# Performance work log

Hardware: AMD Instinct MI355X
Metric: run time of the kernel (lower is better)

Reference implementation:

```python
import jax, jax.numpy as jnp
import numpy as np

INF = 1e8
EPS = 1e-6
STRIDES = (8, 16, 32, 64, 128)
FEAT_SIZES = ((100, 128), (50, 64), (25, 32), (13, 16), (7, 8))
NUM_CLASSES = 81  # args.num_classes + 1
BG = NUM_CLASSES
TOPK1, TOPK2 = 3, 1
RATIO = 0.9
FRACTION = 0.5
B, G = 16, 32
NPER = [h * w for h, w in FEAT_SIZES]
OFFS = np.cumsum([0] + NPER)


def gen_trf():
    j = [2 ** i for i in range(8)]
    r1 = 1 + 6 * j[0]; r2 = r1 + 2 * j[1]
    p2 = r2 + 2 * j[2] * 3; r3 = p2 + 2 * j[2]
    p3 = r3 + 2 * j[3] * 3; r4 = p3 + 2 * j[3]
    p4 = r4 + 2 * j[4] * 5; r5 = p4 + 2 * j[4]
    p5 = r5 + 2 * j[5] * 2
    p6 = p5 + 2 * j[6]; p7 = p6 + 2 * j[7]
    return [p2, p3, p4, p5, p6, p7]


def make_points_rfields():
    trfs = gen_trf()
    pts, rfs = [], []
    for lvl, (h, w) in enumerate(FEAT_SIZES):
        s = STRIDES[lvl]
        xs = jnp.arange(w, dtype=jnp.float32) * s + s // 2
        ys = jnp.arange(h, dtype=jnp.float32) * s + s // 2
        Y, X = jnp.meshgrid(ys, xs, indexing='ij')
        p = jnp.stack([X.reshape(-1), Y.reshape(-1)], -1)
        pts.append(p)
        rf = trfs[lvl + 1] * FRACTION  # fpn_layer == 'p3' -> rfnum = lvl + 1
        rfs.append(jnp.concatenate([p - rf / 2, p + rf / 2], -1))
    return jnp.concatenate(pts, 0), jnp.concatenate(rfs, 0)


def kl_overlaps(gts, anc):
    # BboxDistanceMetric mode='kl': Gaussian KL divergence -> 1/(1+kl); (G, N)
    c1 = (gts[:, :2] + gts[:, 2:]) / 2
    c2 = (anc[:, :2] + anc[:, 2:]) / 2
    w1 = gts[:, 2] - gts[:, 0] + EPS; h1 = gts[:, 3] - gts[:, 1] + EPS
    w2 = anc[:, 2] - anc[:, 0] + EPS; h2 = anc[:, 3] - anc[:, 1] + EPS
    dx = c1[:, None, 0] - c2[None, :, 0]; dy = c1[:, None, 1] - c2[None, :, 1]
    w1s = (w1 ** 2)[:, None]; h1s = (h1 ** 2)[:, None]
    w2s = (w2 ** 2)[None, :]; h2s = (h2 ** 2)[None, :]
    kl = (w2s / w1s + h2s / h1s + 4 * dx ** 2 / w1s + 4 * dy ** 2 / h1s
          + jnp.log(w1s / w2s) + jnp.log(h1s / h2s) - 2) / 2
    return 1.0 / (1.0 + kl)


def hie_assign(rf1, rf2, gts):
    ov1 = kl_overlaps(gts, rf1)
    ov2 = kl_overlaps(gts, rf2)
    N = rf1.shape[0]; Gn = gts.shape[0]
    max_ov = ov1.max(0)
    assigned = jnp.where((max_ov >= 0) & (max_ov < 0.8), 0, -1).astype(jnp.int32)
    gt_ids = jnp.arange(1, Gn + 1, dtype=jnp.int32)
    _, i1 = jax.lax.top_k(ov1, TOPK1)  # (G, k1)
    s1 = jnp.full((N,), -1, jnp.int32).at[i1.reshape(-1)].max(jnp.repeat(gt_ids, TOPK1))
    assigned = jnp.where(s1 > 0, s1, assigned)
    _, i2 = jax.lax.top_k(ov2, TOPK2)  # (G, k2) second hierarchy overrides
    s2 = jnp.full((N,), -1, jnp.int32).at[i2.reshape(-1)].max(jnp.repeat(gt_ids, TOPK2))
    return jnp.where(s2 > 0, s2, assigned)


def target_single(gts, glabels, points, rf1, rf2):
    Gn = gts.shape[0]
    assigned = hie_assign(rf1, rf2, gts)  # (N,) 1-based gt index, 0/-1 = bg
    areas = (gts[:, 2] - gts[:, 0]) * (gts[:, 3] - gts[:, 1])
    mask = (assigned - 1)[:, None] == jnp.arange(Gn)[None, :]
    am = jnp.where(mask, areas[None, :], INF)
    min_area = am.min(1); mi = jnp.argmin(am, 1)
    lab = jnp.where(min_area >= INF, BG, glabels[mi])
    g = gts[mi]
    bt = jnp.stack([points[:, 0] - g[:, 0], points[:, 1] - g[:, 1],
                    g[:, 2] - points[:, 0], g[:, 3] - points[:, 1]], -1)
    return lab, bt


def diou_loss(pred, tgt):
    lt = jnp.maximum(pred[:, :2], tgt[:, :2])
    rb = jnp.minimum(pred[:, 2:], tgt[:, 2:])
    wh = jnp.clip(rb - lt, 0.0)
    ov = wh[:, 0] * wh[:, 1]
    ap = (pred[:, 2] - pred[:, 0]) * (pred[:, 3] - pred[:, 1])
    ag = (tgt[:, 2] - tgt[:, 0]) * (tgt[:, 3] - tgt[:, 1])
    ious = ov / (ap + ag - ov + EPS)
    elt = jnp.minimum(pred[:, :2], tgt[:, :2])
    erb = jnp.maximum(pred[:, 2:], tgt[:, 2:])
    ewh = jnp.clip(erb - elt, 0.0)
    c2 = ewh[:, 0] ** 2 + ewh[:, 1] ** 2 + EPS
    rho2 = ((pred[:, 0] + pred[:, 2] - tgt[:, 0] - tgt[:, 2]) ** 2
            + (pred[:, 1] + pred[:, 3] - tgt[:, 1] - tgt[:, 3]) ** 2) / 4
    return 1.0 - (ious - rho2 / c2)


def _forward(cls_l, bbox_l, ctr_l, gt_bboxes, gt_labels):
    points, rf1 = make_points_rfields()
    c = (rf1[:, :2] + rf1[:, 2:]) / 2
    wh = (rf1[:, 2:] - rf1[:, :2]) * RATIO
    rf2 = jnp.concatenate([c - wh / 2, c + wh / 2], -1)
    labels_all, targets_all = jax.vmap(target_single, (0, 0, None, None, None))(
        gt_bboxes, gt_labels, points, rf1, rf2)
    labels_all = jax.lax.stop_gradient(labels_all)
    targets_all = jax.lax.stop_gradient(targets_all)
    # flatten level-major, image-minor (matches torch.cat order in loss)
    fc = jnp.concatenate([t.transpose(0, 2, 3, 1).reshape(-1, NUM_CLASSES) for t in cls_l], 0)
    fb = jnp.concatenate([t.transpose(0, 2, 3, 1).reshape(-1, 4) for t in bbox_l], 0)
    fo = jnp.concatenate([t.transpose(0, 2, 3, 1).reshape(-1) for t in ctr_l], 0)
    fl = jnp.concatenate([labels_all[:, OFFS[i]:OFFS[i + 1]].reshape(-1) for i in range(5)], 0)
    ft = jnp.concatenate([targets_all[:, OFFS[i]:OFFS[i + 1]].reshape(-1, 4) for i in range(5)], 0)
    fp = jnp.concatenate([jnp.tile(points[OFFS[i]:OFFS[i + 1]], (B, 1)) for i in range(5)], 0)
    pos = fl < BG
    posf = pos.astype(fc.dtype)
    num_pos = jnp.maximum(posf.sum(), 1.0)
    # sigmoid focal loss (alpha=0.25, gamma=2); bg label -> all-zero one-hot
    tgt = jax.nn.one_hot(fl, NUM_CLASSES, dtype=fc.dtype)
    p = jax.nn.sigmoid(fc)
    pt = (1 - p) * tgt + p * (1 - tgt)
    fw = (0.25 * tgt + 0.75 * (1 - tgt)) * pt ** 2
    bce = jnp.maximum(fc, 0) - fc * tgt + jnp.log1p(jnp.exp(-jnp.abs(fc)))
    loss_cls = (bce * fw).sum() / num_pos
    # centerness target (sanitized on negatives to avoid nan)
    bt = jnp.where(pos[:, None], ft, 1.0)
    lr_min = jnp.minimum(bt[:, 0], bt[:, 2]); lr_max = jnp.maximum(bt[:, 0], bt[:, 2])
    tb_min = jnp.minimum(bt[:, 1], bt[:, 3]); tb_max = jnp.maximum(bt[:, 1], bt[:, 3])
    ctr_tgt = jnp.sqrt(jnp.clip((lr_min / lr_max) * (tb_min / tb_max), 0.0)) * posf
    denom = jnp.maximum(ctr_tgt.sum(), 1e-6)
    # decode distances to boxes and DIoU loss weighted by centerness
    x, y = fp[:, 0], fp[:, 1]
    pb = jnp.stack([x - fb[:, 0], y - fb[:, 1], x + fb[:, 2], y + fb[:, 3]], -1)
    tb_box = jnp.stack([x - bt[:, 0], y - bt[:, 1], x + bt[:, 2], y + bt[:, 3]], -1)
    loss_bbox = (diou_loss(pb, tb_box) * ctr_tgt).sum() / denom
    # centerness BCE-with-logits, averaged by num_pos
    bce_c = jnp.maximum(fo, 0) - fo * ctr_tgt + jnp.log1p(jnp.exp(-jnp.abs(fo)))
    loss_ctr = (bce_c * posf).sum() / num_pos
    return jnp.stack([loss_cls, loss_bbox, loss_ctr])


def setup_inputs() -> dict:
    key = jax.random.key(0)
    ks = jax.random.split(key, 24)
    cls_l = [jax.random.normal(ks[i], (B, NUM_CLASSES, h, w), jnp.float32) - 4.0
             for i, (h, w) in enumerate(FEAT_SIZES)]
    bbox_l = [jax.random.uniform(ks[5 + i], (B, 4, h, w), jnp.float32) * 64.0 + 1.0
              for i, (h, w) in enumerate(FEAT_SIZES)]
    ctr_l = [jax.random.normal(ks[10 + i], (B, 1, h, w), jnp.float32)
             for i, (h, w) in enumerate(FEAT_SIZES)]
    cx = jax.random.uniform(ks[15], (B, G)) * 1000.0 + 12.0
    cy = jax.random.uniform(ks[16], (B, G)) * 776.0 + 12.0
    w = jax.random.uniform(ks[17], (B, G)) * 240.0 + 8.0
    h = jax.random.uniform(ks[18], (B, G)) * 240.0 + 8.0
    gt_bboxes = jnp.stack([cx - w / 2, cy - h / 2, cx + w / 2, cy + h / 2], -1)
    gt_labels = jax.random.randint(ks[19], (B, G), 0, 80)
    d = {}
    for i in range(5):
        d[f'cls{i}'] = cls_l[i]; d[f'bbox{i}'] = bbox_l[i]; d[f'ctr{i}'] = ctr_l[i]
    d['gt_bboxes'] = gt_bboxes
    d['gt_labels'] = gt_labels
    return d


def reference(cls0, cls1, cls2, cls3, cls4, bbox0, bbox1, bbox2, bbox3, bbox4,
              ctr0, ctr1, ctr2, ctr3, ctr4, gt_bboxes, gt_labels):
    return _forward([cls0, cls1, cls2, cls3, cls4],
                    [bbox0, bbox1, bbox2, bbox3, bbox4],
                    [ctr0, ctr1, ctr2, ctr3, ctr4], gt_bboxes, gt_labels)
```

## Files before the change

kernel.cpp:

```cpp
#include <hip/hip_runtime.h>
#include <math.h>
#include <limits.h>

#pragma clang fp contract(off)

#define N_ANCH 17064
#define BATCH  16
#define NGT    32
#define BG_CLS 81
#define EPSF   1e-6f

#define NPB     512
#define NSTREAM 2048
#define L2E 1.44269504088896340736f
#define LN2 0.69314718055994530942f

#define F4_0 4147200
#define C1   4147200
#define C2   5184000
#define C3   5443200
#define C4   5510592
#define TOT4 5528736

__device__ __forceinline__ float fexp2(float x){ return __builtin_amdgcn_exp2f(x); }
__device__ __forceinline__ float flog2(float x){ return __builtin_amdgcn_logf(x); }
__device__ __forceinline__ float frcp (float x){ return __builtin_amdgcn_rcpf(x); }

struct Geo { int lvl; int j; int HW; float px; float py; };

__device__ __forceinline__ Geo geom(int n) {
  Geo g;
  if (n < 12800)      { g.lvl=0; g.j=n;       g.HW=12800; g.px=(float)((g.j & 127)*8 + 4);   g.py=(float)((g.j >> 7)*8 + 4);   }
  else if (n < 16000) { g.lvl=1; g.j=n-12800; g.HW=3200;  g.px=(float)((g.j & 63)*16 + 8);   g.py=(float)((g.j >> 6)*16 + 8);  }
  else if (n < 16800) { g.lvl=2; g.j=n-16000; g.HW=800;   g.px=(float)((g.j & 31)*32 + 16);  g.py=(float)((g.j >> 5)*32 + 16); }
  else if (n < 17008) { g.lvl=3; g.j=n-16800; g.HW=208;   g.px=(float)((g.j & 15)*64 + 32);  g.py=(float)((g.j >> 4)*64 + 32); }
  else                { g.lvl=4; g.j=n-17008; g.HW=56;    g.px=(float)((g.j & 7)*128 + 64);  g.py=(float)((g.j >> 3)*128 + 64);}
  return g;
}

__device__ __forceinline__ bool bet(float av, int ai, float bv, int bi) {
  return (av < bv) || (av == bv && ai < bi);
}

__device__ __forceinline__ void insert3min(float* v, int* i, float nv, int ni) {
  if (nv < v[0])      { v[2]=v[1]; i[2]=i[1]; v[1]=v[0]; i[1]=i[0]; v[0]=nv; i[0]=ni; }
  else if (nv < v[1]) { v[2]=v[1]; i[2]=i[1]; v[1]=nv; i[1]=ni; }
  else                { v[2]=nv; i[2]=ni; }
}

__device__ __forceinline__ void insert3tie(float* v, int* i, float nv, int ni) {
  if (!bet(nv, ni, v[2], i[2])) return;
  if (bet(nv, ni, v[0], i[0]))      { v[2]=v[1]; i[2]=i[1]; v[1]=v[0]; i[1]=i[0]; v[0]=nv; i[0]=ni; }
  else if (bet(nv, ni, v[1], i[1])) { v[2]=v[1]; i[2]=i[1]; v[1]=nv; i[1]=ni; }
  else                              { v[2]=nv; i[2]=ni; }
}

__device__ __forceinline__ float negterm(float x) {
  float ax = fabsf(x);
  float e  = fexp2(ax * -L2E);
  float r  = frcp(1.0f + e);
  float p  = (x >= 0.0f) ? r : e * r;
  float sp = fmaxf(x, 0.0f) + flog2(1.0f + e) * LN2;
  return 0.75f * (p * p) * sp;
}

__global__ __launch_bounds__(256) void megaK(const float4* __restrict__ gtb,
                                             const float4* __restrict__ s0,
                                             const float4* __restrict__ s1,
                                             const float4* __restrict__ s2,
                                             const float4* __restrict__ s3,
                                             const float4* __restrict__ s4,
                                             int4* __restrict__ win,
                                             float* __restrict__ part) {
  __shared__ float sv[256 * 3];
  __shared__ int   si[256 * 3];
  __shared__ float tv[256];
  __shared__ int   ti[256];
  __shared__ float sh[256];

  int t = threadIdx.x;
  if (blockIdx.x < NPB) {
    int blk = blockIdx.x;
    int b = blk >> 5, g = blk & 31;
    float4 GB = gtb[b * NGT + g];
    float c1x = (GB.x + GB.z) * 0.5f, c1y = (GB.y + GB.w) * 0.5f;
    float w1 = GB.z - GB.x + EPSF, h1 = GB.w - GB.y + EPSF;
    float w1s = w1 * w1, h1s = h1 * h1;
    float iw = 1.0f / w1s, ih = 1.0f / h1s;
    float iws = iw + ih;
    float Lg = logf(w1s) + logf(h1s);
    float Ay = 4.0f * ih;
    float Axc = 4.0f * iw;

    float v1[3] = {INFINITY, INFINITY, INFINITY};
    int   i1[3] = {INT_MAX, INT_MAX, INT_MAX};
    float v2 = INFINITY; int i2 = INT_MAX;

    #define DO_LEVEL(BASE, LGW, H, STRIDE, RF) do {                             \
      const int W_ = 1 << (LGW);                                                \
      float w2a = (RF) + 1e-6f;          float w2sa = w2a * w2a;                \
      float w2b = (RF) * 0.9f + 1e-6f;   float w2sb = w2b * w2b;                \
      float K1 = w2sa * iws + Lg - 2.0f * logf(w2sa) - 2.0f;                    \
      float K2 = w2sb * iws + Lg - 2.0f * logf(w2sb) - 2.0f;                    \
      int col = t & (W_ - 1);                                                   \
      float px = (float)(col * (STRIDE) + (STRIDE) / 2);                        \
      float dx = c1x - px;                                                      \
      float kx1 = Axc * dx * dx + K1;                                           \
      float kx2 = Axc * dx * dx + K2;                                           \
      int rstep = 256 >> (LGW);                                                 \
      for (int row = t >> (LGW); row < (H); row += rstep) {                     \
        float py = (float)(row * (STRIDE) + (STRIDE) / 2);                      \
        float dy = c1y - py;                                                    \
        float dy2 = dy * dy;                                                    \
        float k1 = fmaf(Ay, dy2, kx1);                                          \
        float k2 = fmaf(Ay, dy2, kx2);                                          \
        int n = (BASE) + (row << (LGW)) + col;                                  \
        if (k1 < v1[2]) insert3min(v1, i1, k1, n);                              \
        if (k2 < v2) { v2 = k2; i2 = n; }                                       \
      }                                                                         \
    } while (0)

    DO_LEVEL(0,     7, 100,   8,  45.5f);
    DO_LEVEL(12800, 6,  50,  16, 133.5f);
    DO_LEVEL(16000, 5,  25,  32, 213.5f);
    DO_LEVEL(16800, 4,  13,  64, 277.5f);
    DO_LEVEL(17008, 3,   7, 128, 405.5f);
    #undef DO_LEVEL

    sv[t*3+0] = v1[0]; sv[t*3+1] = v1[1]; sv[t*3+2] = v1[2];
    si[t*3+0] = i1[0]; si[t*3+1] = i1[1]; si[t*3+2] = i1[2];
    tv[t] = v2; ti[t] = i2;
    __syncthreads();
    for (int off = 128; off > 0; off >>= 1) {
      if (t < off) {
        #pragma unroll
        for (int k = 0; k < 3; ++k)
          insert3tie(&sv[t * 3], &si[t * 3], sv[(t + off) * 3 + k], si[(t + off) * 3 + k]);
        if (bet(tv[t + off], ti[t + off], tv[t], ti[t])) { tv[t] = tv[t + off]; ti[t] = ti[t + off]; }
      }
      __syncthreads();
    }
    if (t == 0) win[blk] = make_int4(si[0], si[1], si[2], ti[0]);
  } else {
    int sb = blockIdx.x - NPB;
    float local = 0.0f;
    for (int i = sb * 256 + t; i < TOT4; i += NSTREAM * 256) {
      const float4* p; int off;
      if (i < C1)      { p = s0; off = i; }
      else if (i < C2) { p = s1; off = i - C1; }
      else if (i < C3) { p = s2; off = i - C2; }
      else if (i < C4) { p = s3; off = i - C3; }
      else             { p = s4; off = i - C4; }
      float4 f = p[off];
      local += negterm(f.x);
      local += negterm(f.y);
      local += negterm(f.z);
      local += negterm(f.w);
    }
    sh[t] = local;
    __syncthreads();
    #pragma unroll
    for (int off = 128; off > 0; off >>= 1) {
      if (t < off) sh[t] += sh[t + off];
      __syncthreads();
    }
    if (t == 0) part[sb] = sh[0];
  }
}

__global__ __launch_bounds__(1024) void resolveK(
    const int* __restrict__ win, const float4* __restrict__ gtb, const int* __restrict__ glab,
    const float* __restrict__ c0, const float* __restrict__ c1, const float* __restrict__ c2,
    const float* __restrict__ c3, const float* __restrict__ c4,
    const float* __restrict__ bb0, const float* __restrict__ bb1, const float* __restrict__ bb2,
    const float* __restrict__ bb3, const float* __restrict__ bb4,
    const float* __restrict__ ct0, const float* __restrict__ ct1, const float* __restrict__ ct2,
    const float* __restrict__ ct3, const float* __restrict__ ct4,
    const float* __restrict__ part, float* __restrict__ out) {
  int t = threadIdx.x;
  __shared__ unsigned int keys[NPB * 4];
  for (int k = t; k < NPB * 4; k += 1024) {
    int blk = k >> 2, s = k & 3;
    int b = blk >> 5, g = blk & 31;
    int n = win[k];
    unsigned int pri = ((s == 3) ? 32u : 0u) + (unsigned int)g;
    keys[k] = (((unsigned int)(b * 32768 + n)) << 6) | pri;
  }
  __syncthreads();

  double a_cls = 0.0, a_pos = 0.0, a_ctr = 0.0, a_diou = 0.0, a_cbce = 0.0;

  for (int i = t; i < NSTREAM; i += 1024) a_cls += (double)part[i];

  const float* clsA[5] = {c0, c1, c2, c3, c4};
  const float* bbA[5]  = {bb0, bb1, bb2, bb3, bb4};
  const float* ctA[5]  = {ct0, ct1, ct2, ct3, ct4};

  for (int k = t; k < NPB * 4; k += 1024) {
    unsigned int me = keys[k];
    unsigned int bn = me >> 6;
    int b = (int)(bn >> 15);
    int base = b * 128;
    bool alive = true;
    #pragma unroll 4
    for (int j = 0; j < 128; ++j) {
      unsigned int o = keys[base + j];
      if ((o >> 6) == bn && o > me) { alive = false; }
    }
    if (!alive) continue;

    int n = (int)(bn & 32767u);
    int g = (int)(me & 31u);
    int lab = glab[b * NGT + g];
    float4 gb = gtb[b * NGT + g];
    Geo G = geom(n);

    const float* bb = bbA[G.lvl];
    const float* ct = ctA[G.lvl];
    const float* cp = clsA[G.lvl];

    const float* bp = bb + b * 4 * G.HW + G.j;
    float f0 = bp[0];
    float f1 = bp[G.HW];
    float f2 = bp[2 * G.HW];
    float f3 = bp[3 * G.HW];
    float fo = ct[b * G.HW + G.j];
    float xc = cp[((size_t)(b * 81 + lab)) * G.HW + G.j];

    {
      float ax = fabsf(xc);
      float e  = fexp2(ax * -L2E);
      float r  = frcp(1.0f + e);
      float p  = (xc >= 0.0f) ? r : e * r;
      float sp = fmaxf(xc, 0.0f) + flog2(1.0f + e) * LN2;
      float neg = 0.75f * (p * p) * sp;
      float omp = 1.0f - p;
      float pos = 0.25f * (omp * omp) * (sp - xc);
      a_cls += (double)(pos - neg);
    }

    float tx = G.px - gb.x, ty = G.py - gb.y, tz = gb.z - G.px, tw = gb.w - G.py;

    float lr_min = fminf(tx, tz), lr_max = fmaxf(tx, tz);
    float tb_min = fminf(ty, tw), tb_max = fmaxf(ty, tw);
    float prod = (lr_min / lr_max) * (tb_min / tb_max);
    float ctrt = sqrtf(fmaxf(prod, 0.0f));

    float pb0 = G.px - f0, pb1 = G.py - f1, pb2 = G.px + f2, pb3 = G.py + f3;
    float tb0 = G.px - tx, tb1 = G.py - ty, tb2 = G.px + tz, tb3 = G.py + tw;

    float ltx = fmaxf(pb0, tb0), lty = fmaxf(pb1, tb1);
    float rbx = fminf(pb2, tb2), rby = fminf(pb3, tb3);
    float whx = fmaxf(rbx - ltx, 0.0f), why = fmaxf(rby - lty, 0.0f);
    float ovl = whx * why;
    float ap = (pb2 - pb0) * (pb3 - pb1);
    float ag = (tb2 - tb0) * (tb3 - tb1);
    float ious = ovl / (ap + ag - ovl + EPSF);
    float eltx = fminf(pb0, tb0), elty = fminf(pb1, tb1);
    float erbx = fmaxf(pb2, tb2), erby = fmaxf(pb3, tb3);
    float ewx = fmaxf(erbx - eltx, 0.0f), ewy = fmaxf(erby - elty, 0.0f);
    float c2v = ewx * ewx + ewy * ewy + EPSF;
    float sx = pb0 + pb2 - tb0 - tb2;
    float sy = pb1 + pb3 - tb1 - tb3;
    float rho2 = (sx * sx + sy * sy) * 0.25f;
    float dl = 1.0f - (ious - rho2 / c2v);

    a_pos  += 1.0;
    a_ctr  += (double)ctrt;
    a_diou += (double)(dl * ctrt);
    a_cbce += (double)(fmaxf(fo, 0.0f) - fo * ctrt + log1pf(expf(-fabsf(fo))));
  }

  __shared__ double r0[1024], r1[1024], r2[1024], r3[1024], r4[1024];
  r0[t] = a_cls; r1[t] = a_pos; r2[t] = a_ctr; r3[t] = a_diou; r4[t] = a_cbce;
  __syncthreads();
  #pragma unroll
  for (int off = 512; off > 0; off >>= 1) {
    if (t < off) {
      r0[t] += r0[t + off]; r1[t] += r1[t + off]; r2[t] += r2[t + off];
      r3[t] += r3[t + off]; r4[t] += r4[t + off];
    }
    __syncthreads();
  }
  if (t == 0) {
    double np_ = r1[0] > 1.0 ? r1[0] : 1.0;
    double dn  = r2[0] > 1e-6 ? r2[0] : 1e-6;
    out[0] = (float)(r0[0] / np_);
    out[1] = (float)(r3[0] / dn);
    out[2] = (float)(r4[0] / np_);
  }
}

extern "C" void kernel_launch(void* const* d_in, const int* in_sizes, int n_in,
                              void* d_out, int out_size, void* d_ws, size_t ws_size,
                              hipStream_t stream) {
  (void)in_sizes; (void)n_in; (void)out_size; (void)ws_size;
  const float* cls[5] = {(const float*)d_in[0],  (const float*)d_in[3],  (const float*)d_in[6],
                         (const float*)d_in[9],  (const float*)d_in[12]};
  const float* bbx[5] = {(const float*)d_in[1],  (const float*)d_in[4],  (const float*)d_in[7],
                         (const float*)d_in[10], (const float*)d_in[13]};
  const float* ctr[5] = {(const float*)d_in[2],  (const float*)d_in[5],  (const float*)d_in[8],
                         (const float*)d_in[11], (const float*)d_in[14]};
  const float4* gtb = (const float4*)d_in[15];
  const int* glab = (const int*)d_in[16];

  char* ws = (char*)d_ws;
  int4*  win  = (int4*)ws;
  float* part = (float*)(ws + NPB * 16);

  megaK<<<NPB + NSTREAM, 256, 0, stream>>>(gtb,
                                           (const float4*)cls[0], (const float4*)cls[1],
                                           (const float4*)cls[2], (const float4*)cls[3],
                                           (const float4*)cls[4],
                                           win, part);
  resolveK<<<1, 1024, 0, stream>>>((const int*)win, gtb, glab,
                                   cls[0], cls[1], cls[2], cls[3], cls[4],
                                   bbx[0], bbx[1], bbx[2], bbx[3], bbx[4],
                                   ctr[0], ctr[1], ctr[2], ctr[3], ctr[4],
                                   part, (float*)d_out);
}
```

Measured before the change: 42.79 us.

## Split resolve kernel into per-batch blocks with last-block final reduction

The single 1024-thread resolve kernel is replaced by one 256-thread block per batch image. Each block deduplicates its own 128 winner keys and computes the positive-anchor losses, then publishes per-batch partial sums through atomics. A done-counter, reset inside the first kernel, lets the last finishing block sum the stream partials and write the final outputs. This spreads the serial resolve work across several compute units, at the cost of atomic coordination and a counter-ordering dependency between the two kernels.

```diff
diff --git a/kernel.cpp b/kernel.cpp
--- a/kernel.cpp
+++ b/kernel.cpp
@@ -15,7 +15,6 @@
 #define L2E 1.44269504088896340736f
 #define LN2 0.69314718055994530942f
 
-#define F4_0 4147200
 #define C1   4147200
 #define C2   5184000
 #define C3   5443200
@@ -71,7 +70,8 @@
                                              const float4* __restrict__ s3,
                                              const float4* __restrict__ s4,
                                              int4* __restrict__ win,
-                                             float* __restrict__ part) {
+                                             float* __restrict__ part,
+                                             int* __restrict__ done) {
   __shared__ float sv[256 * 3];
   __shared__ int   si[256 * 3];
   __shared__ float tv[256];
@@ -79,6 +79,8 @@
   __shared__ float sh[256];
 
   int t = threadIdx.x;
+  if (blockIdx.x == 0 && t == 0) *done = 0;
+
   if (blockIdx.x < NPB) {
     int blk = blockIdx.x;
     int b = blk >> 5, g = blk & 31;
@@ -168,7 +170,7 @@
   }
 }
 
-__global__ __launch_bounds__(1024) void resolveK(
+__global__ __launch_bounds__(256) void resolveK(
     const int* __restrict__ win, const float4* __restrict__ gtb, const int* __restrict__ glab,
     const float* __restrict__ c0, const float* __restrict__ c1, const float* __restrict__ c2,
     const float* __restrict__ c3, const float* __restrict__ c4,
@@ -176,118 +178,150 @@
     const float* __restrict__ bb3, const float* __restrict__ bb4,
     const float* __restrict__ ct0, const float* __restrict__ ct1, const float* __restrict__ ct2,
     const float* __restrict__ ct3, const float* __restrict__ ct4,
-    const float* __restrict__ part, float* __restrict__ out) {
+    const float* __restrict__ part,
+    unsigned long long* __restrict__ bpart,
+    int* __restrict__ done,
+    float* __restrict__ out) {
   int t = threadIdx.x;
-  __shared__ unsigned int keys[NPB * 4];
-  for (int k = t; k < NPB * 4; k += 1024) {
-    int blk = k >> 2, s = k & 3;
-    int b = blk >> 5, g = blk & 31;
-    int n = win[k];
+  int b = blockIdx.x;
+  __shared__ unsigned int ukeys[128];
+
+  if (t < 128) {
+    int g = t >> 2, s = t & 3;
+    int n = win[(b * NGT + g) * 4 + s];
     unsigned int pri = ((s == 3) ? 32u : 0u) + (unsigned int)g;
-    keys[k] = (((unsigned int)(b * 32768 + n)) << 6) | pri;
+    ukeys[t] = (((unsigned int)n) << 6) | pri;
   }
   __syncthreads();
 
   double a_cls = 0.0, a_pos = 0.0, a_ctr = 0.0, a_diou = 0.0, a_cbce = 0.0;
-
-  for (int i = t; i < NSTREAM; i += 1024) a_cls += (double)part[i];
 
   const float* clsA[5] = {c0, c1, c2, c3, c4};
   const float* bbA[5]  = {bb0, bb1, bb2, bb3, bb4};
   const float* ctA[5]  = {ct0, ct1, ct2, ct3, ct4};
 
-  for (int k = t; k < NPB * 4; k += 1024) {
-    unsigned int me = keys[k];
-    unsigned int bn = me >> 6;
-    int b = (int)(bn >> 15);
-    int base = b * 128;
+  if (t < 128) {
+    unsigned int me = ukeys[t];
+    unsigned int nn = me >> 6;
     bool alive = true;
-    #pragma unroll 4
+    #pragma unroll 8
     for (int j = 0; j < 128; ++j) {
-      unsigned int o = keys[base + j];
-      if ((o >> 6) == bn && o > me) { alive = false; }
-    }
-    if (!alive) continue;
-
-    int n = (int)(bn & 32767u);
-    int g = (int)(me & 31u);
-    int lab = glab[b * NGT + g];
-    float4 gb = gtb[b * NGT + g];
-    Geo G = geom(n);
-
-    const float* bb = bbA[G.lvl];
-    const float* ct = ctA[G.lvl];
-    const float* cp = clsA[G.lvl];
-
-    const float* bp = bb + b * 4 * G.HW + G.j;
-    float f0 = bp[0];
-    float f1 = bp[G.HW];
-    float f2 = bp[2 * G.HW];
-    float f3 = bp[3 * G.HW];
-    float fo = ct[b * G.HW + G.j];
-    float xc = cp[((size_t)(b * 81 + lab)) * G.HW + G.j];
-
-    {
-      float ax = fabsf(xc);
-      float e  = fexp2(ax * -L2E);
-      float r  = frcp(1.0f + e);
-      float p  = (xc >= 0.0f) ? r : e * r;
-      float sp = fmaxf(xc, 0.0f) + flog2(1.0f + e) * LN2;
-      float neg = 0.75f * (p * p) * sp;
-      float omp = 1.0f - p;
-      float pos = 0.25f * (omp * omp) * (sp - xc);
-      a_cls += (double)(pos - neg);
-    }
-
-    float tx = G.px - gb.x, ty = G.py - gb.y, tz = gb.z - G.px, tw = gb.w - G.py;
-
-    float lr_min = fminf(tx, tz), lr_max = fmaxf(tx, tz);
-    float tb_min = fminf(ty, tw), tb_max = fmaxf(ty, tw);
-    float prod = (lr_min / lr_max) * (tb_min / tb_max);
-    float ctrt = sqrtf(fmaxf(prod, 0.0f));
-
-    float pb0 = G.px - f0, pb1 = G.py - f1, pb2 = G.px + f2, pb3 = G.py + f3;
-    float tb0 = G.px - tx, tb1 = G.py - ty, tb2 = G.px + tz, tb3 = G.py + tw;
-
-    float ltx = fmaxf(pb0, tb0), lty = fmaxf(pb1, tb1);
-    float rbx = fminf(pb2, tb2), rby = fminf(pb3, tb3);
-    float whx = fmaxf(rbx - ltx, 0.0f), why = fmaxf(rby - lty, 0.0f);
-    float ovl = whx * why;
-    float ap = (pb2 - pb0) * (pb3 - pb1);
-    float ag = (tb2 - tb0) * (tb3 - tb1);
-    float ious = ovl / (ap + ag - ovl + EPSF);
-    float eltx = fminf(pb0, tb0), elty = fminf(pb1, tb1);
-    float erbx = fmaxf(pb2, tb2), erby = fmaxf(pb3, tb3);
-    float ewx = fmaxf(erbx - eltx, 0.0f), ewy = fmaxf(erby - elty, 0.0f);
-    float c2v = ewx * ewx + ewy * ewy + EPSF;
-    float sx = pb0 + pb2 - tb0 - tb2;
-    float sy = pb1 + pb3 - tb1 - tb3;
-    float rho2 = (sx * sx + sy * sy) * 0.25f;
-    float dl = 1.0f - (ious - rho2 / c2v);
-
-    a_pos  += 1.0;
-    a_ctr  += (double)ctrt;
-    a_diou += (double)(dl * ctrt);
-    a_cbce += (double)(fmaxf(fo, 0.0f) - fo * ctrt + log1pf(expf(-fabsf(fo))));
-  }
-
-  __shared__ double r0[1024], r1[1024], r2[1024], r3[1024], r4[1024];
+      unsigned int o = ukeys[j];
+      if ((o >> 6) == nn && o > me) alive = false;
+    }
+    if (alive) {
+      int n = (int)nn;
+      int g = (int)(me & 31u);
+      int lab = glab[b * NGT + g];
+      float4 gb = gtb[b * NGT + g];
+      Geo G = geom(n);
+
+      const float* bb = bbA[G.lvl];
+      const float* ct = ctA[G.lvl];
+      const float* cp = clsA[G.lvl];
+
+      const float* bp = bb + b * 4 * G.HW + G.j;
+      float f0 = bp[0];
+      float f1 = bp[G.HW];
+      float f2 = bp[2 * G.HW];
+      float f3 = bp[3 * G.HW];
+      float fo = ct[b * G.HW + G.j];
+      float xc = cp[((size_t)(b * 81 + lab)) * G.HW + G.j];
+
+      {
+        float ax = fabsf(xc);
+        float e  = fexp2(ax * -L2E);
+        float r  = frcp(1.0f + e);
+        float p  = (xc >= 0.0f) ? r : e * r;
+        float sp = fmaxf(xc, 0.0f) + flog2(1.0f + e) * LN2;
+        float neg = 0.75f * (p * p) * sp;
+        float omp = 1.0f - p;
+        float pos = 0.25f * (omp * omp) * (sp - xc);
+        a_cls += (double)(pos - neg);
+      }
+
+      float tx = G.px - gb.x, ty = G.py - gb.y, tz = gb.z - G.px, tw = gb.w - G.py;
+
+      float lr_min = fminf(tx, tz), lr_max = fmaxf(tx, tz);
+      float tb_min = fminf(ty, tw), tb_max = fmaxf(ty, tw);
+      float prod = (lr_min / lr_max) * (tb_min / tb_max);
+      float ctrt = sqrtf(fmaxf(prod, 0.0f));
+
+      float pb0 = G.px - f0, pb1 = G.py - f1, pb2 = G.px + f2, pb3 = G.py + f3;
+      float tb0 = G.px - tx, tb1 = G.py - ty, tb2 = G.px + tz, tb3 = G.py + tw;
+
+      float ltx = fmaxf(pb0, tb0), lty = fmaxf(pb1, tb1);
+      float rbx = fminf(pb2, tb2), rby = fminf(pb3, tb3);
+      float whx = fmaxf(rbx - ltx, 0.0f), why = fmaxf(rby - lty, 0.0f);
+      float ovl = whx * why;
+      float ap = (pb2 - pb0) * (pb3 - pb1);
+      float ag = (tb2 - tb0) * (tb3 - tb1);
+      float ious = ovl / (ap + ag - ovl + EPSF);
+      float eltx = fminf(pb0, tb0), elty = fminf(pb1, tb1);
+      float erbx = fmaxf(pb2, tb2), erby = fmaxf(pb3, tb3);
+      float ewx = fmaxf(erbx - eltx, 0.0f), ewy = fmaxf(erby - elty, 0.0f);
+      float c2v = ewx * ewx + ewy * ewy + EPSF;
+      float sx = pb0 + pb2 - tb0 - tb2;
+      float sy = pb1 + pb3 - tb1 - tb3;
+      float rho2 = (sx * sx + sy * sy) * 0.25f;
+      float dl = 1.0f - (ious - rho2 / c2v);
+
+      a_pos  += 1.0;
+      a_ctr  += (double)ctrt;
+      a_diou += (double)(dl * ctrt);
+      a_cbce += (double)(fmaxf(fo, 0.0f) - fo * ctrt + log1pf(expf(-fabsf(fo))));
+    }
+  }
+
+  __shared__ double r0[256], r1[256], r2[256], r3[256], r4[256];
   r0[t] = a_cls; r1[t] = a_pos; r2[t] = a_ctr; r3[t] = a_diou; r4[t] = a_cbce;
   __syncthreads();
   #pragma unroll
-  for (int off = 512; off > 0; off >>= 1) {
+  for (int off = 128; off > 0; off >>= 1) {
     if (t < off) {
       r0[t] += r0[t + off]; r1[t] += r1[t + off]; r2[t] += r2[t + off];
       r3[t] += r3[t + off]; r4[t] += r4[t + off];
     }
     __syncthreads();
   }
+
+  __shared__ int lastFlag;
   if (t == 0) {
-    double np_ = r1[0] > 1.0 ? r1[0] : 1.0;
-    double dn  = r2[0] > 1e-6 ? r2[0] : 1e-6;
-    out[0] = (float)(r0[0] / np_);
-    out[1] = (float)(r3[0] / dn);
-    out[2] = (float)(r4[0] / np_);
+    atomicExch(&bpart[b * 5 + 0], __double_as_longlong(r0[0]));
+    atomicExch(&bpart[b * 5 + 1], __double_as_longlong(r1[0]));
+    atomicExch(&bpart[b * 5 + 2], __double_as_longlong(r2[0]));
+    atomicExch(&bpart[b * 5 + 3], __double_as_longlong(r3[0]));
+    atomicExch(&bpart[b * 5 + 4], __double_as_longlong(r4[0]));
+    __threadfence();
+    int old = atomicAdd(done, 1);
+    lastFlag = (old == BATCH - 1) ? 1 : 0;
+  }
+  __syncthreads();
+  if (!lastFlag) return;
+
+  double c = 0.0;
+  for (int i = t; i < NSTREAM; i += 256) c += (double)part[i];
+  r0[t] = c;
+  __syncthreads();
+  #pragma unroll
+  for (int off = 128; off > 0; off >>= 1) {
+    if (t < off) r0[t] += r0[t + off];
+    __syncthreads();
+  }
+  if (t == 0) {
+    double sc = r0[0], sp = 0.0, sct = 0.0, sdi = 0.0, scb = 0.0;
+    for (int i = 0; i < BATCH; ++i) {
+      sc  += __longlong_as_double(atomicAdd(&bpart[i * 5 + 0], 0ull));
+      sp  += __longlong_as_double(atomicAdd(&bpart[i * 5 + 1], 0ull));
+      sct += __longlong_as_double(atomicAdd(&bpart[i * 5 + 2], 0ull));
+      sdi += __longlong_as_double(atomicAdd(&bpart[i * 5 + 3], 0ull));
+      scb += __longlong_as_double(atomicAdd(&bpart[i * 5 + 4], 0ull));
+    }
+    double np_ = sp > 1.0 ? sp : 1.0;
+    double dn  = sct > 1e-6 ? sct : 1e-6;
+    out[0] = (float)(sc / np_);
+    out[1] = (float)(sdi / dn);
+    out[2] = (float)(scb / np_);
   }
 }
 
@@ -307,15 +341,17 @@
   char* ws = (char*)d_ws;
   int4*  win  = (int4*)ws;
   float* part = (float*)(ws + NPB * 16);
+  int*   done = (int*)(ws + 16384);
+  unsigned long long* bpart = (unsigned long long*)(ws + 16448);
 
   megaK<<<NPB + NSTREAM, 256, 0, stream>>>(gtb,
                                            (const float4*)cls[0], (const float4*)cls[1],
                                            (const float4*)cls[2], (const float4*)cls[3],
                                            (const float4*)cls[4],
-                                           win, part);
-  resolveK<<<1, 1024, 0, stream>>>((const int*)win, gtb, glab,
-                                   cls[0], cls[1], cls[2], cls[3], cls[4],
-                                   bbx[0], bbx[1], bbx[2], bbx[3], bbx[4],
-                                   ctr[0], ctr[1], ctr[2], ctr[3], ctr[4],
-                                   part, (float*)d_out);
-}
+                                           win, part, done);
+  resolveK<<<BATCH, 256, 0, stream>>>((const int*)win, gtb, glab,
+                                      cls[0], cls[1], cls[2], cls[3], cls[4],
+                                      bbx[0], bbx[1], bbx[2], bbx[3], bbx[4],
+                                      ctr[0], ctr[1], ctr[2], ctr[3], ctr[4],
+                                      part, bpart, done, (float*)d_out);
+}
```

Result: slower. 45.85 us (+7.1%).
